# Performance work log

Hardware: AMD Instinct MI355X
Metric: run time of the kernel (lower is better)

The kernel has to match this reference:

```python
import jax, jax.numpy as jnp
import numpy as np
from jax import lax

PAD_IDX = 0
SOS_IDX = 1


def gru_cell(x, h, w_ih, w_hh, b_ih, b_hh):
    # PyTorch GRU cell: gates ordered [r, z, n]
    gi = x @ w_ih.T + b_ih            # [B, 3H]
    gh = h @ w_hh.T + b_hh            # [B, 3H]
    i_r, i_z, i_n = jnp.split(gi, 3, axis=-1)
    h_r, h_z, h_n = jnp.split(gh, 3, axis=-1)
    r = jax.nn.sigmoid(i_r + h_r)
    z = jax.nn.sigmoid(i_z + h_z)
    n = jnp.tanh(i_n + r * h_n)
    return (1.0 - z) * n + z * h


def setup_inputs() -> dict:
    key = jax.random.key(0)
    ks = jax.random.split(key, 24)
    B, S, T = 32, 64, 48
    Vs, Vt, E, H = 32000, 32000, 512, 1024
    sH = 1.0 / np.sqrt(H)
    sE = 1.0 / np.sqrt(E)

    def p(k, shape, scale):
        return jax.random.normal(k, shape, jnp.float32) * scale

    inp = {
        'source_ids': jax.random.randint(ks[0], (B, S), 0, Vs),
        'target_ids': jax.random.randint(ks[1], (B, T), 0, Vt),
        'enc_embed': p(ks[2], (Vs, E), 0.02).at[PAD_IDX].set(0.0),
        'enc_w_ih': p(ks[3], (3 * H, E), sE),
        'enc_w_hh': p(ks[4], (3 * H, H), sH),
        'enc_b_ih': p(ks[5], (3 * H,), sH),
        'enc_b_hh': p(ks[6], (3 * H,), sH),
        'wq': p(ks[7], (H, H), sH),
        'bq': p(ks[8], (H,), sH),
        'wk': p(ks[9], (H, H), sH),
        'bk': p(ks[10], (H,), sH),
        'ws': p(ks[11], (H,), sH),
        'bs': p(ks[12], (), sH),
        'dec_embed': p(ks[13], (Vt, E), 0.02).at[PAD_IDX].set(0.0),
        'dec_w_ih': p(ks[14], (3 * H, E + H), sH),
        'dec_w_hh': p(ks[15], (3 * H, H), sH),
        'dec_b_ih': p(ks[16], (3 * H,), sH),
        'dec_b_hh': p(ks[17], (3 * H,), sH),
        'wo': p(ks[18], (Vt, H), sH),
        'bo': p(ks[19], (Vt,), sH),
    }
    return inp


def reference(source_ids, target_ids, enc_embed, enc_w_ih, enc_w_hh, enc_b_ih,
              enc_b_hh, wq, bq, wk, bk, ws, bs, dec_embed, dec_w_ih, dec_w_hh,
              dec_b_ih, dec_b_hh, wo, bo):
    B, S = source_ids.shape
    T = target_ids.shape[1]
    H = wq.shape[0]

    # ----- encoder GRU -----
    enc_emb = enc_embed[source_ids]                  # [B,S,E] (dropout = identity, eval)
    h0 = jnp.zeros((B, H), enc_emb.dtype)

    def enc_step(h, x):
        h = gru_cell(x, h, enc_w_ih, enc_w_hh, enc_b_ih, enc_b_hh)
        return h, h

    h_final, enc_out = lax.scan(enc_step, h0, enc_emb.transpose(1, 0, 2))
    enc_out = enc_out.transpose(1, 0, 2)             # [B,S,H]

    mask = source_ids != PAD_IDX                     # [B,S]
    keys_proj = enc_out @ wk.T + bk                  # [B,S,H] (hoisted; linear, step-invariant)

    # ----- decoder with teacher forcing (ratio=1.0 => always teacher) -----
    dec_in = jnp.concatenate(
        [jnp.full((B, 1), SOS_IDX, dtype=target_ids.dtype), target_ids[:, 1:T - 1]],
        axis=1)                                      # [B,T-1]
    dec_emb = dec_embed[dec_in].transpose(1, 0, 2)   # [T-1,B,E]

    def dec_step(h, emb):
        q = h @ wq.T + bq                            # [B,H]
        scores = jnp.tanh(q[:, None, :] + keys_proj) @ ws + bs   # [B,S]
        scores = jnp.where(mask, scores, -jnp.inf)
        w = jax.nn.softmax(scores, axis=-1)          # [B,S]
        ctx = jnp.einsum('bs,bsh->bh', w, enc_out)   # [B,H]
        x = jnp.concatenate([emb, ctx], axis=-1)     # [B,E+H]
        h2 = gru_cell(x, h, dec_w_ih, dec_w_hh, dec_b_ih, dec_b_hh)
        logits = h2 @ wo.T + bo                      # [B,V]
        return h2, (logits, w)

    _, (logits, attn) = lax.scan(dec_step, h_final, dec_emb)
    logits = logits.transpose(1, 0, 2)               # [B,T-1,V]
    attn = attn.transpose(1, 0, 2)                   # [B,T-1,S]
    return logits, attn
```

## Files before the change

kernel.cpp:

```cpp
#include <hip/hip_runtime.h>


#define BB 32
#define SS 64
#define TT 48
#define TD 47
#define EE 512
#define HH 1024
#define GG 3072
#define VV 32000
#define SOS_IDX 1
#define MPAD 1536

typedef float f32x4 __attribute__((ext_vector_type(4)));
typedef short bf16x8 __attribute__((ext_vector_type(8)));

static __device__ __forceinline__ float sigmoid_f(float x) {
    return 1.0f / (1.0f + __expf(-x));
}
static __device__ __forceinline__ float tanh_f(float x) {
    return 1.0f - 2.0f / (__expf(2.0f * x) + 1.0f);
}
static __device__ __forceinline__ unsigned short f2bf(float f) {
    unsigned u = __float_as_uint(f);
    u = u + 0x7fffu + ((u >> 16) & 1u);
    return (unsigned short)(u >> 16);
}

__global__ void k_dec_idx(const int* __restrict__ tgt, int* __restrict__ idx) {
    int m = blockIdx.x * 256 + threadIdx.x;
    if (m < TD * BB) {
        int t = m >> 5, b = m & 31;
        idx[m] = (t == 0) ? SOS_IDX : tgt[b * TT + t];
    }
}

__global__ __launch_bounds__(256) void k_gemm128(
    const float* __restrict__ A, const float* __restrict__ Wt,
    const float* __restrict__ bias, float* __restrict__ C,
    const int* __restrict__ rowidx,
    int M, int N, int K, int lda, int ldw, int ldc)
{
    __shared__ __align__(16) float As[16][128];
    __shared__ __align__(16) float Bs[16][128];
    const int tid = threadIdx.x;
    const int tm = tid >> 4, tn = tid & 15;
    const int row0 = blockIdx.y * 128;
    const int col0 = blockIdx.x * 128;
    const int lr = tid >> 1;
    const int lq = tid & 1;

    long arow_off = -1;
    {
        int arow = row0 + lr;
        if (arow < M) {
            int r = rowidx ? rowidx[arow] : arow;
            arow_off = (long)r * lda;
        }
    }
    const long wrow_off = (long)(col0 + lr) * ldw;

    float acc[8][8];
#pragma unroll
    for (int i = 0; i < 8; ++i)
#pragma unroll
        for (int j = 0; j < 8; ++j) acc[i][j] = 0.f;

    for (int k0 = 0; k0 < K; k0 += 16) {
        f32x4 av0 = {0.f,0.f,0.f,0.f}, av1 = {0.f,0.f,0.f,0.f};
        if (arow_off >= 0) {
            av0 = *(const f32x4*)(A + arow_off + k0 + lq * 8);
            av1 = *(const f32x4*)(A + arow_off + k0 + lq * 8 + 4);
        }
        f32x4 wv0 = *(const f32x4*)(Wt + wrow_off + k0 + lq * 8);
        f32x4 wv1 = *(const f32x4*)(Wt + wrow_off + k0 + lq * 8 + 4);
        __syncthreads();
#pragma unroll
        for (int i = 0; i < 4; ++i) {
            As[lq * 8 + i][lr] = av0[i];
            As[lq * 8 + 4 + i][lr] = av1[i];
            Bs[lq * 8 + i][lr] = wv0[i];
            Bs[lq * 8 + 4 + i][lr] = wv1[i];
        }
        __syncthreads();
#pragma unroll
        for (int kk = 0; kk < 16; ++kk) {
            f32x4 a0 = *(const f32x4*)&As[kk][tm * 4];
            f32x4 a1 = *(const f32x4*)&As[kk][64 + tm * 4];
            f32x4 b0 = *(const f32x4*)&Bs[kk][tn * 4];
            f32x4 b1 = *(const f32x4*)&Bs[kk][64 + tn * 4];
            float a[8], b[8];
#pragma unroll
            for (int i = 0; i < 4; ++i) {
                a[i] = a0[i]; a[4 + i] = a1[i];
                b[i] = b0[i]; b[4 + i] = b1[i];
            }
#pragma unroll
            for (int i = 0; i < 8; ++i)
#pragma unroll
                for (int j = 0; j < 8; ++j) acc[i][j] += a[i] * b[j];
        }
    }

    f32x4 bv0 = {0.f,0.f,0.f,0.f}, bv1 = {0.f,0.f,0.f,0.f};
    if (bias) {
        bv0 = *(const f32x4*)(bias + col0 + tn * 4);
        bv1 = *(const f32x4*)(bias + col0 + 64 + tn * 4);
    }
#pragma unroll
    for (int i = 0; i < 8; ++i) {
        int m = row0 + ((i < 4) ? (tm * 4 + i) : (64 + tm * 4 + i - 4));
        if (m >= M) continue;
        f32x4 v0, v1;
#pragma unroll
        for (int j = 0; j < 4; ++j) {
            v0[j] = acc[i][j] + bv0[j];
            v1[j] = acc[i][4 + j] + bv1[j];
        }
        *(f32x4*)(C + (long)m * ldc + col0 + tn * 4) = v0;
        *(f32x4*)(C + (long)m * ldc + col0 + 64 + tn * 4) = v1;
    }
}

__global__ __launch_bounds__(256) void k_cvtA(
    const float* __restrict__ A, unsigned short* __restrict__ Ah,
    unsigned short* __restrict__ Al)
{
    size_t i4 = ((size_t)blockIdx.x * 256 + threadIdx.x) * 4;
    int row = (int)(i4 >> 10);
    f32x4 v = {0.f, 0.f, 0.f, 0.f};
    if (row < TD * BB) v = *(const f32x4*)(A + i4);
    ushort4 h, l;
    float hf;
    h.x = f2bf(v.x); hf = __uint_as_float((unsigned)h.x << 16); l.x = f2bf(v.x - hf);
    h.y = f2bf(v.y); hf = __uint_as_float((unsigned)h.y << 16); l.y = f2bf(v.y - hf);
    h.z = f2bf(v.z); hf = __uint_as_float((unsigned)h.z << 16); l.z = f2bf(v.z - hf);
    h.w = f2bf(v.w); hf = __uint_as_float((unsigned)h.w << 16); l.w = f2bf(v.w - hf);
    *(ushort4*)(Ah + i4) = h;
    *(ushort4*)(Al + i4) = l;
}

__global__ __launch_bounds__(256) void k_cvtB(
    const float* __restrict__ Bsrc, unsigned short* __restrict__ Bh)
{
    size_t i4 = ((size_t)blockIdx.x * 256 + threadIdx.x) * 4;
    f32x4 v = *(const f32x4*)(Bsrc + i4);
    ushort4 h;
    h.x = f2bf(v.x); h.y = f2bf(v.y); h.z = f2bf(v.z); h.w = f2bf(v.w);
    *(ushort4*)(Bh + i4) = h;
}

__global__ __launch_bounds__(256) void k_mfma_logits(
    const unsigned short* __restrict__ Ah,
    const unsigned short* __restrict__ Bh,
    const float* __restrict__ bo, float* __restrict__ C)
{
    __shared__ __align__(16) unsigned short As[128 * 64];
    __shared__ __align__(16) unsigned short Bs[128 * 64];
    const int tid = threadIdx.x;
    const int m0 = blockIdx.y * 128;
    const int n0 = blockIdx.x * 128;
    const int r = tid >> 1, half = tid & 1;
    const int lane = tid & 63, wid = tid >> 6;
    const int wm = wid >> 1, wn = wid & 1;

    f32x4 acc[4][4];
#pragma unroll
    for (int i = 0; i < 4; ++i)
#pragma unroll
        for (int j = 0; j < 4; ++j) acc[i][j] = (f32x4){0.f, 0.f, 0.f, 0.f};

    char* AsB = (char*)As;
    char* BsB = (char*)Bs;
    const int lwb = r * 128 + half * 64;
    const int swz = (r & 7) << 4;

    for (int kt = 0; kt < 32; ++kt) {
        const int kb = (kt & 15) * 64;
        const unsigned short* Ap = Ah + ((kt >> 4) ? (size_t)MPAD * 1024 : 0)
                                 + (size_t)(m0 + r) * 1024 + kb + half * 32;
        const unsigned short* Bp = Bh + (size_t)(n0 + r) * 1024 + kb + half * 32;
        f32x4 a0 = *(const f32x4*)(Ap + 0);
        f32x4 a1 = *(const f32x4*)(Ap + 8);
        f32x4 a2 = *(const f32x4*)(Ap + 16);
        f32x4 a3 = *(const f32x4*)(Ap + 24);
        f32x4 b0 = *(const f32x4*)(Bp + 0);
        f32x4 b1 = *(const f32x4*)(Bp + 8);
        f32x4 b2 = *(const f32x4*)(Bp + 16);
        f32x4 b3 = *(const f32x4*)(Bp + 24);
        __syncthreads();
        *(f32x4*)(AsB + ((lwb + 0)  ^ swz)) = a0;
        *(f32x4*)(AsB + ((lwb + 16) ^ swz)) = a1;
        *(f32x4*)(AsB + ((lwb + 32) ^ swz)) = a2;
        *(f32x4*)(AsB + ((lwb + 48) ^ swz)) = a3;
        *(f32x4*)(BsB + ((lwb + 0)  ^ swz)) = b0;
        *(f32x4*)(BsB + ((lwb + 16) ^ swz)) = b1;
        *(f32x4*)(BsB + ((lwb + 32) ^ swz)) = b2;
        *(f32x4*)(BsB + ((lwb + 48) ^ swz)) = b3;
        __syncthreads();
#pragma unroll
        for (int ks = 0; ks < 2; ++ks) {
            bf16x8 af[4], bf[4];
#pragma unroll
            for (int u = 0; u < 4; ++u) {
                int ml = wm * 64 + u * 16 + (lane & 15);
                int byteA = ml * 128 + ks * 64 + ((lane >> 4) << 4);
                af[u] = *(const bf16x8*)(AsB + (byteA ^ ((ml & 7) << 4)));
                int nl = wn * 64 + u * 16 + (lane & 15);
                int byteB = nl * 128 + ks * 64 + ((lane >> 4) << 4);
                bf[u] = *(const bf16x8*)(BsB + (byteB ^ ((nl & 7) << 4)));
            }
#pragma unroll
            for (int mi = 0; mi < 4; ++mi)
#pragma unroll
                for (int ni = 0; ni < 4; ++ni)
                    acc[mi][ni] = __builtin_amdgcn_mfma_f32_16x16x32_bf16(
                        af[mi], bf[ni], acc[mi][ni], 0, 0, 0);
        }
    }

    const int cl = lane & 15, rq = lane >> 4;
#pragma unroll
    for (int ni = 0; ni < 4; ++ni) {
        int col = n0 + wn * 64 + ni * 16 + cl;
        float bias = bo[col];
#pragma unroll
        for (int mi = 0; mi < 4; ++mi) {
#pragma unroll
            for (int j = 0; j < 4; ++j) {
                int m = m0 + wm * 64 + mi * 16 + rq * 4 + j;
                if (m < TD * BB) {
                    int orow = (m & 31) * TD + (m >> 5);
                    C[(size_t)orow * VV + col] = acc[mi][ni][j] + bias;
                }
            }
        }
    }
}

__global__ __launch_bounds__(512, 2) void k_enc_step(
    const float* __restrict__ gi, const float* __restrict__ Whh,
    const float* __restrict__ bhh, float* __restrict__ enc_out, int s)
{
    __shared__ float red[12][16][32];
    __shared__ float sums[12][32];
    const int tid = threadIdx.x, bid = blockIdx.x;
    const int b = tid & 31, ks = tid >> 5;
    const int j0 = bid * 4;
    const int kc = ks * 64;

    float acc[12];
#pragma unroll
    for (int u = 0; u < 12; ++u) acc[u] = 0.f;
    if (s > 0) {
        f32x4 hreg[16];
        const float* hb = enc_out + ((size_t)b * SS + (s - 1)) * HH + kc;
#pragma unroll
        for (int i = 0; i < 16; ++i) hreg[i] = *(const f32x4*)(hb + (i << 2));
#pragma unroll
        for (int jj = 0; jj < 4; ++jj) {
            const float* pr = Whh + ((size_t)(j0 + jj) << 10) + kc;
            const float* pz = Whh + ((size_t)(HH + j0 + jj) << 10) + kc;
            const float* pn = Whh + ((size_t)(2 * HH + j0 + jj) << 10) + kc;
            float ar = 0.f, az = 0.f, an = 0.f;
#pragma unroll
            for (int i = 0; i < 16; ++i) {
                f32x4 h4 = hreg[i];
                f32x4 w;
                w = *(const f32x4*)(pr + (i << 2));
                ar += h4.x * w.x + h4.y * w.y + h4.z * w.z + h4.w * w.w;
                w = *(const f32x4*)(pz + (i << 2));
                az += h4.x * w.x + h4.y * w.y + h4.z * w.z + h4.w * w.w;
                w = *(const f32x4*)(pn + (i << 2));
                an += h4.x * w.x + h4.y * w.y + h4.z * w.z + h4.w * w.w;
            }
            acc[jj] = ar; acc[4 + jj] = az; acc[8 + jj] = an;
        }
    }
#pragma unroll
    for (int u = 0; u < 12; ++u) red[u][ks][b] = acc[u];
    __syncthreads();
    if (tid < 384) {
        int u = tid >> 5, fb = tid & 31;
        float x = 0.f;
#pragma unroll
        for (int q = 0; q < 16; ++q) x += red[u][q][fb];
        sums[u][fb] = x;
    }
    __syncthreads();
    if (tid < 32) {
        const f32x4 bh0 = *(const f32x4*)(bhh + j0);
        const f32x4 bh1 = *(const f32x4*)(bhh + HH + j0);
        const f32x4 bh2 = *(const f32x4*)(bhh + 2 * HH + j0);
        const float* gr = gi + (size_t)(tid * SS + s) * GG;
        f32x4 g0 = *(const f32x4*)(gr + j0);
        f32x4 g1 = *(const f32x4*)(gr + HH + j0);
        f32x4 g2 = *(const f32x4*)(gr + 2 * HH + j0);
        f32x4 hold = {0.f, 0.f, 0.f, 0.f};
        if (s > 0) hold = *(const f32x4*)(enc_out + ((size_t)tid * SS + (s - 1)) * HH + j0);
        f32x4 hn;
#pragma unroll
        for (int e = 0; e < 4; ++e) {
            float r = sigmoid_f(g0[e] + sums[e][tid] + bh0[e]);
            float z = sigmoid_f(g1[e] + sums[4 + e][tid] + bh1[e]);
            float n = tanh_f(g2[e] + r * (sums[8 + e][tid] + bh2[e]));
            hn[e] = (1.f - z) * n + z * hold[e];
        }
        *(f32x4*)(enc_out + ((size_t)tid * SS + s) * HH + j0) = hn;
    }
}

__global__ __launch_bounds__(512, 2) void k_hq(
    const float* __restrict__ hbase, long hstride,
    const float* __restrict__ Whh, const float* __restrict__ wq,
    const float* __restrict__ bq, float* __restrict__ qbuf,
    float* __restrict__ hsums)
{
    __shared__ float red[16][16][32];
    __shared__ float qsum[4][32];
    const int tid = threadIdx.x, bid = blockIdx.x;
    const int b = tid & 31, ks = tid >> 5;
    const int j0 = bid * 4;
    const int kc = ks * 64;

    f32x4 hreg[16];
    const float* hb = hbase + (size_t)b * hstride + kc;
#pragma unroll
    for (int i = 0; i < 16; ++i) hreg[i] = *(const f32x4*)(hb + (i << 2));
    float acc[16];
#pragma unroll
    for (int jj = 0; jj < 4; ++jj) {
        const float* pr = Whh + ((size_t)(j0 + jj) << 10) + kc;
        const float* pz = Whh + ((size_t)(HH + j0 + jj) << 10) + kc;
        const float* pn = Whh + ((size_t)(2 * HH + j0 + jj) << 10) + kc;
        const float* pq = wq + ((size_t)(j0 + jj) << 10) + kc;
        float ar = 0.f, az = 0.f, an = 0.f, aq = 0.f;
#pragma unroll
        for (int i = 0; i < 16; ++i) {
            f32x4 h4 = hreg[i];
            f32x4 w;
            w = *(const f32x4*)(pr + (i << 2));
            ar += h4.x * w.x + h4.y * w.y + h4.z * w.z + h4.w * w.w;
            w = *(const f32x4*)(pz + (i << 2));
            az += h4.x * w.x + h4.y * w.y + h4.z * w.z + h4.w * w.w;
            w = *(const f32x4*)(pn + (i << 2));
            an += h4.x * w.x + h4.y * w.y + h4.z * w.z + h4.w * w.w;
            w = *(const f32x4*)(pq + (i << 2));
            aq += h4.x * w.x + h4.y * w.y + h4.z * w.z + h4.w * w.w;
        }
        acc[jj] = ar; acc[4 + jj] = az; acc[8 + jj] = an; acc[12 + jj] = aq;
    }
#pragma unroll
    for (int u = 0; u < 16; ++u) red[u][ks][b] = acc[u];
    __syncthreads();
    {
        int u = tid >> 5, fb = tid & 31;
        float x = 0.f;
#pragma unroll
        for (int q = 0; q < 16; ++q) x += red[u][q][fb];
        if (u < 12) {
            int g = u >> 2, jj = u & 3;
            hsums[(size_t)g * BB * HH + (size_t)fb * HH + j0 + jj] = x;
        } else {
            qsum[u - 12][fb] = x;
        }
    }
    __syncthreads();
    if (tid < 32) {
        const f32x4 bq4 = *(const f32x4*)(bq + j0);
        f32x4 qv;
        qv.x = qsum[0][tid] + bq4.x;
        qv.y = qsum[1][tid] + bq4.y;
        qv.z = qsum[2][tid] + bq4.z;
        qv.w = qsum[3][tid] + bq4.w;
        *(f32x4*)(qbuf + (size_t)tid * HH + j0) = qv;
    }
}

__global__ __launch_bounds__(512, 2) void k_attn_fin(
    const float* __restrict__ qbuf, const float* __restrict__ keys,
    const float* __restrict__ wsv, const float* __restrict__ bsv,
    const int* __restrict__ src, const float* __restrict__ encproj,
    const float* __restrict__ gi, const float* __restrict__ bhh,
    const float* __restrict__ hsums, const float* __restrict__ hbase,
    long hstride, float* __restrict__ h2all, float* __restrict__ attn_out,
    int t)
{
    __shared__ float qs[HH];
    __shared__ float wss[HH];
    __shared__ float sc[8][64];
    __shared__ float wl[64];
    __shared__ float xls[GG];
    const int ab = blockIdx.x;
    const int tid = threadIdx.x;
    if (tid < 256) {
        *(f32x4*)&qs[tid * 4] = *(const f32x4*)(qbuf + (size_t)ab * HH + tid * 4);
        *(f32x4*)&wss[tid * 4] = *(const f32x4*)(wsv + tid * 4);
    }
    __syncthreads();
    {
        const int s4 = tid >> 3, kq = tid & 7;
        const float* kr = keys + (size_t)(ab * SS + s4) * HH + kq * 128;
        float a = 0.f;
        for (int i = 0; i < 32; ++i) {
            f32x4 kv = *(const f32x4*)(kr + (i << 2));
            int k = kq * 128 + (i << 2);
            a += tanh_f(qs[k] + kv.x) * wss[k]
               + tanh_f(qs[k + 1] + kv.y) * wss[k + 1]
               + tanh_f(qs[k + 2] + kv.z) * wss[k + 2]
               + tanh_f(qs[k + 3] + kv.w) * wss[k + 3];
        }
        sc[kq][s4] = a;
    }
    __syncthreads();
    if (tid < 64) {
        float v = bsv[0];
#pragma unroll
        for (int q = 0; q < 8; ++q) v += sc[q][tid];
        bool valid = src[ab * SS + tid] != 0;
        float m = valid ? v : -3.0e38f;
        for (int off = 32; off; off >>= 1) m = fmaxf(m, __shfl_xor(m, off));
        float e = valid ? __expf(v - m) : 0.f;
        float ssum = e;
        for (int off = 32; off; off >>= 1) ssum += __shfl_xor(ssum, off);
        float wgt = e / ssum;
        wl[tid] = wgt;
        attn_out[((size_t)ab * TD + t) * SS + tid] = wgt;
    }
    __syncthreads();
    {
        float xa[6] = {0.f, 0.f, 0.f, 0.f, 0.f, 0.f};
        for (int s2 = 0; s2 < SS; ++s2) {
            float wgt = wl[s2];
            const float* ep = encproj + (size_t)(ab * SS + s2) * GG;
#pragma unroll
            for (int u = 0; u < 6; ++u)
                xa[u] += wgt * ep[u * 512 + tid];
        }
#pragma unroll
        for (int u = 0; u < 6; ++u) xls[u * 512 + tid] = xa[u];
    }
    __syncthreads();
    const float* gr = gi + (size_t)(t * BB + ab) * GG;
#pragma unroll
    for (int half = 0; half < 2; ++half) {
        int j = half * 512 + tid;
        float g0 = gr[j] + xls[j];
        float g1 = gr[HH + j] + xls[HH + j];
        float g2 = gr[2 * HH + j] + xls[2 * HH + j];
        float sh0 = hsums[(size_t)0 * BB * HH + (size_t)ab * HH + j];
        float sh1 = hsums[(size_t)1 * BB * HH + (size_t)ab * HH + j];
        float sh2 = hsums[(size_t)2 * BB * HH + (size_t)ab * HH + j];
        float r = sigmoid_f(g0 + sh0 + bhh[j]);
        float z = sigmoid_f(g1 + sh1 + bhh[HH + j]);
        float n = tanh_f(g2 + r * (sh2 + bhh[2 * HH + j]));
        float hold = hbase[(size_t)ab * hstride + j];
        h2all[((size_t)t * BB + ab) * HH + j] = (1.f - z) * n + z * hold;
    }
}

extern "C" void kernel_launch(void* const* d_in, const int* in_sizes, int n_in,
                              void* d_out, int out_size, void* d_ws, size_t ws_size,
                              hipStream_t stream)
{
    const int*   src  = (const int*)d_in[0];
    const int*   tgt  = (const int*)d_in[1];
    const float* eemb = (const float*)d_in[2];
    const float* ewih = (const float*)d_in[3];
    const float* ewhh = (const float*)d_in[4];
    const float* ebih = (const float*)d_in[5];
    const float* ebhh = (const float*)d_in[6];
    const float* wq   = (const float*)d_in[7];
    const float* bq   = (const float*)d_in[8];
    const float* wk   = (const float*)d_in[9];
    const float* bk   = (const float*)d_in[10];
    const float* wsv  = (const float*)d_in[11];
    const float* bsv  = (const float*)d_in[12];
    const float* demb = (const float*)d_in[13];
    const float* dwih = (const float*)d_in[14];
    const float* dwhh = (const float*)d_in[15];
    const float* dbih = (const float*)d_in[16];
    const float* dbhh = (const float*)d_in[17];
    const float* wo   = (const float*)d_in[18];
    const float* bo   = (const float*)d_in[19];
    float* out = (float*)d_out;

    float* w = (float*)d_ws;
    float* enc_gi  = w;
    float* dec_gi  = enc_gi  + (size_t)BB * SS * GG;
    float* enc_out = dec_gi  + (size_t)TD * BB * GG;
    float* keys    = enc_out + (size_t)BB * SS * HH;
    float* h2all   = keys    + (size_t)BB * SS * HH;
    float* qbuf    = h2all   + (size_t)TD * BB * HH;
    float* hsums   = qbuf    + (size_t)BB * HH;
    int*   didx    = (int*)(hsums + (size_t)3 * BB * HH);
    unsigned short* Ah = (unsigned short*)(didx + TD * BB + 32);
    unsigned short* Al = Ah + (size_t)MPAD * 1024;
    unsigned short* Bh = (unsigned short*)w;

    float* encproj = enc_gi;
    float* attn_out = out + (size_t)BB * TD * VV;

    k_dec_idx<<<dim3((TD * BB + 255) / 256), 256, 0, stream>>>(tgt, didx);

    k_gemm128<<<dim3(GG / 128, (BB * SS) / 128), 256, 0, stream>>>(
        eemb, ewih, ebih, enc_gi, src, BB * SS, GG, EE, EE, EE, GG);
    k_gemm128<<<dim3(GG / 128, (TD * BB + 127) / 128), 256, 0, stream>>>(
        demb, dwih, dbih, dec_gi, didx, TD * BB, GG, EE, EE, EE + HH, GG);

    for (int s = 0; s < SS; ++s)
        k_enc_step<<<dim3(256), dim3(512), 0, stream>>>(
            enc_gi, ewhh, ebhh, enc_out, s);

    k_gemm128<<<dim3(HH / 128, (BB * SS) / 128), 256, 0, stream>>>(
        enc_out, wk, bk, keys, nullptr, BB * SS, HH, HH, HH, HH, HH);
    k_gemm128<<<dim3(GG / 128, (BB * SS) / 128), 256, 0, stream>>>(
        enc_out, dwih + EE, nullptr, encproj, nullptr,
        BB * SS, GG, HH, HH, EE + HH, GG);

    for (int t = 0; t < TD; ++t) {
        const float* hbase = (t == 0) ? enc_out + (size_t)(SS - 1) * HH
                                      : h2all + (size_t)(t - 1) * BB * HH;
        long hstride = (t == 0) ? (long)SS * HH : (long)HH;
        k_hq<<<dim3(256), dim3(512), 0, stream>>>(
            hbase, hstride, dwhh, wq, bq, qbuf, hsums);
        k_attn_fin<<<dim3(BB), dim3(512), 0, stream>>>(
            qbuf, keys, wsv, bsv, src, encproj, dec_gi, dbhh, hsums,
            hbase, hstride, h2all, attn_out, t);
    }

    k_cvtA<<<dim3(MPAD * 1024 / 1024), 256, 0, stream>>>(h2all, Ah, Al);
    k_cvtB<<<dim3(VV * 1024 / 1024), 256, 0, stream>>>(wo, Bh);
    k_mfma_logits<<<dim3(VV / 128, MPAD / 128), 256, 0, stream>>>(
        Ah, Bh, bo, out);
}
```

Measured before the change: 4.495 ms.

## Fuse recurrent steps with software grid barriers and merge decoder kernels

Batches four encoder GRU steps per launch, separated by a hierarchical atomic grid barrier, which cuts the encoder from 64 launches to 16. The decoder's two per-step kernels (h/q projection and attention+GRU finish) become one 256-block kernel with a grid barrier between them. The attention and gate stage is spread over 256 blocks instead of 32: each block handles one batch row and a 128-column slice, and the softmax is recomputed redundantly in every slice. Cross-block stores use sc0/sc1 cache-bypassing instructions for coherence. The barrier relies on all 256 blocks being co-resident, and deadlocks if they are not.

```diff
diff --git a/kernel.cpp b/kernel.cpp
--- a/kernel.cpp
+++ b/kernel.cpp
@@ -25,6 +25,31 @@
     unsigned u = __float_as_uint(f);
     u = u + 0x7fffu + ((u >> 16) & 1u);
     return (unsigned short)(u >> 16);
+}
+static __device__ __forceinline__ void cst4(float* p, f32x4 v) {
+    asm volatile("global_store_dwordx4 %0, %1, off sc0 sc1" :: "v"(p), "v"(v) : "memory");
+}
+static __device__ __forceinline__ void cst1(float* p, float v) {
+    asm volatile("global_store_dword %0, %1, off sc0 sc1" :: "v"(p), "v"(v) : "memory");
+}
+
+static __device__ __forceinline__ void gbar(int* bar, int leafsz, int& bstep) {
+    asm volatile("s_waitcnt vmcnt(0) lgkmcnt(0)" ::: "memory");
+    __syncthreads();
+    bstep += 1;
+    if (threadIdx.x == 0) {
+        int* leaf = bar + (blockIdx.x & 7) * 32;
+        int* root = bar + 512;
+        int lv = __hip_atomic_fetch_add(leaf, 1, __ATOMIC_RELAXED, __HIP_MEMORY_SCOPE_AGENT) + 1;
+        if (lv == bstep * leafsz) {
+            __hip_atomic_fetch_add(root, 1, __ATOMIC_RELAXED, __HIP_MEMORY_SCOPE_AGENT);
+        }
+        while (__hip_atomic_load(root, __ATOMIC_RELAXED, __HIP_MEMORY_SCOPE_AGENT) < bstep * 8) {
+            __builtin_amdgcn_s_sleep(1);
+        }
+    }
+    __syncthreads();
+    asm volatile("" ::: "memory");
 }
 
 __global__ void k_dec_idx(const int* __restrict__ tgt, int* __restrict__ idx) {
@@ -238,9 +263,10 @@
     }
 }
 
-__global__ __launch_bounds__(512, 2) void k_enc_step(
+__global__ __launch_bounds__(512, 2) void k_enc_steps(
     const float* __restrict__ gi, const float* __restrict__ Whh,
-    const float* __restrict__ bhh, float* __restrict__ enc_out, int s)
+    const float* __restrict__ bhh, float* __restrict__ enc_out,
+    int s0, int ns, int* bar)
 {
     __shared__ float red[12][16][32];
     __shared__ float sums[12][32];
@@ -248,21 +274,105 @@
     const int b = tid & 31, ks = tid >> 5;
     const int j0 = bid * 4;
     const int kc = ks * 64;
-
-    float acc[12];
-#pragma unroll
-    for (int u = 0; u < 12; ++u) acc[u] = 0.f;
-    if (s > 0) {
+    int bstep = 0;
+
+    for (int ss = 0; ss < ns; ++ss) {
+        const int s = s0 + ss;
+        float acc[12];
+#pragma unroll
+        for (int u = 0; u < 12; ++u) acc[u] = 0.f;
+        if (s > 0) {
+            f32x4 hreg[16];
+            const float* hb = enc_out + ((size_t)b * SS + (s - 1)) * HH + kc;
+#pragma unroll
+            for (int i = 0; i < 16; ++i) hreg[i] = *(const f32x4*)(hb + (i << 2));
+#pragma unroll
+            for (int jj = 0; jj < 4; ++jj) {
+                const float* pr = Whh + ((size_t)(j0 + jj) << 10) + kc;
+                const float* pz = Whh + ((size_t)(HH + j0 + jj) << 10) + kc;
+                const float* pn = Whh + ((size_t)(2 * HH + j0 + jj) << 10) + kc;
+                float ar = 0.f, az = 0.f, an = 0.f;
+#pragma unroll
+                for (int i = 0; i < 16; ++i) {
+                    f32x4 h4 = hreg[i];
+                    f32x4 w;
+                    w = *(const f32x4*)(pr + (i << 2));
+                    ar += h4.x * w.x + h4.y * w.y + h4.z * w.z + h4.w * w.w;
+                    w = *(const f32x4*)(pz + (i << 2));
+                    az += h4.x * w.x + h4.y * w.y + h4.z * w.z + h4.w * w.w;
+                    w = *(const f32x4*)(pn + (i << 2));
+                    an += h4.x * w.x + h4.y * w.y + h4.z * w.z + h4.w * w.w;
+                }
+                acc[jj] = ar; acc[4 + jj] = az; acc[8 + jj] = an;
+            }
+        }
+#pragma unroll
+        for (int u = 0; u < 12; ++u) red[u][ks][b] = acc[u];
+        __syncthreads();
+        if (tid < 384) {
+            int u = tid >> 5, fb = tid & 31;
+            float x = 0.f;
+#pragma unroll
+            for (int q = 0; q < 16; ++q) x += red[u][q][fb];
+            sums[u][fb] = x;
+        }
+        __syncthreads();
+        if (tid < 32) {
+            const f32x4 bh0 = *(const f32x4*)(bhh + j0);
+            const f32x4 bh1 = *(const f32x4*)(bhh + HH + j0);
+            const f32x4 bh2 = *(const f32x4*)(bhh + 2 * HH + j0);
+            const float* gr = gi + (size_t)(tid * SS + s) * GG;
+            f32x4 g0 = *(const f32x4*)(gr + j0);
+            f32x4 g1 = *(const f32x4*)(gr + HH + j0);
+            f32x4 g2 = *(const f32x4*)(gr + 2 * HH + j0);
+            f32x4 hold = {0.f, 0.f, 0.f, 0.f};
+            if (s > 0) hold = *(const f32x4*)(enc_out + ((size_t)tid * SS + (s - 1)) * HH + j0);
+            f32x4 hn;
+#pragma unroll
+            for (int e = 0; e < 4; ++e) {
+                float r = sigmoid_f(g0[e] + sums[e][tid] + bh0[e]);
+                float z = sigmoid_f(g1[e] + sums[4 + e][tid] + bh1[e]);
+                float n = tanh_f(g2[e] + r * (sums[8 + e][tid] + bh2[e]));
+                hn[e] = (1.f - z) * n + z * hold[e];
+            }
+            cst4(enc_out + ((size_t)tid * SS + s) * HH + j0, hn);
+        }
+        if (ss != ns - 1) gbar(bar, 256 / 8, bstep);
+    }
+}
+
+__global__ __launch_bounds__(512, 2) void k_dec_step(
+    const float* __restrict__ hbase, long hstride,
+    const float* __restrict__ Whh, const float* __restrict__ wq,
+    const float* __restrict__ bq, const float* __restrict__ keys,
+    const float* __restrict__ wsv, const float* __restrict__ bsv,
+    const int* __restrict__ src, const float* __restrict__ encproj,
+    const float* __restrict__ gi, const float* __restrict__ bhh,
+    float* __restrict__ q2, float* __restrict__ hsums2,
+    float* __restrict__ h2all, float* __restrict__ attn_out,
+    int t, int* bar)
+{
+    __shared__ float red[16][16][32];
+    __shared__ float qsum[4][32];
+    const int tid = threadIdx.x, bid = blockIdx.x;
+    const int b = tid & 31, ks = tid >> 5;
+    const int j0 = bid * 4;
+    const int kc = ks * 64;
+    int bstep = 0;
+
+    {
         f32x4 hreg[16];
-        const float* hb = enc_out + ((size_t)b * SS + (s - 1)) * HH + kc;
+        const float* hb = hbase + (size_t)b * hstride + kc;
 #pragma unroll
         for (int i = 0; i < 16; ++i) hreg[i] = *(const f32x4*)(hb + (i << 2));
+        float acc[16];
 #pragma unroll
         for (int jj = 0; jj < 4; ++jj) {
             const float* pr = Whh + ((size_t)(j0 + jj) << 10) + kc;
             const float* pz = Whh + ((size_t)(HH + j0 + jj) << 10) + kc;
             const float* pn = Whh + ((size_t)(2 * HH + j0 + jj) << 10) + kc;
-            float ar = 0.f, az = 0.f, an = 0.f;
+            const float* pq = wq + ((size_t)(j0 + jj) << 10) + kc;
+            float ar = 0.f, az = 0.f, an = 0.f, aq = 0.f;
 #pragma unroll
             for (int i = 0; i < 16; ++i) {
                 f32x4 h4 = hreg[i];
@@ -273,129 +383,46 @@
                 az += h4.x * w.x + h4.y * w.y + h4.z * w.z + h4.w * w.w;
                 w = *(const f32x4*)(pn + (i << 2));
                 an += h4.x * w.x + h4.y * w.y + h4.z * w.z + h4.w * w.w;
+                w = *(const f32x4*)(pq + (i << 2));
+                aq += h4.x * w.x + h4.y * w.y + h4.z * w.z + h4.w * w.w;
             }
-            acc[jj] = ar; acc[4 + jj] = az; acc[8 + jj] = an;
-        }
-    }
-#pragma unroll
-    for (int u = 0; u < 12; ++u) red[u][ks][b] = acc[u];
-    __syncthreads();
-    if (tid < 384) {
-        int u = tid >> 5, fb = tid & 31;
-        float x = 0.f;
-#pragma unroll
-        for (int q = 0; q < 16; ++q) x += red[u][q][fb];
-        sums[u][fb] = x;
-    }
-    __syncthreads();
-    if (tid < 32) {
-        const f32x4 bh0 = *(const f32x4*)(bhh + j0);
-        const f32x4 bh1 = *(const f32x4*)(bhh + HH + j0);
-        const f32x4 bh2 = *(const f32x4*)(bhh + 2 * HH + j0);
-        const float* gr = gi + (size_t)(tid * SS + s) * GG;
-        f32x4 g0 = *(const f32x4*)(gr + j0);
-        f32x4 g1 = *(const f32x4*)(gr + HH + j0);
-        f32x4 g2 = *(const f32x4*)(gr + 2 * HH + j0);
-        f32x4 hold = {0.f, 0.f, 0.f, 0.f};
-        if (s > 0) hold = *(const f32x4*)(enc_out + ((size_t)tid * SS + (s - 1)) * HH + j0);
-        f32x4 hn;
-#pragma unroll
-        for (int e = 0; e < 4; ++e) {
-            float r = sigmoid_f(g0[e] + sums[e][tid] + bh0[e]);
-            float z = sigmoid_f(g1[e] + sums[4 + e][tid] + bh1[e]);
-            float n = tanh_f(g2[e] + r * (sums[8 + e][tid] + bh2[e]));
-            hn[e] = (1.f - z) * n + z * hold[e];
-        }
-        *(f32x4*)(enc_out + ((size_t)tid * SS + s) * HH + j0) = hn;
-    }
-}
-
-__global__ __launch_bounds__(512, 2) void k_hq(
-    const float* __restrict__ hbase, long hstride,
-    const float* __restrict__ Whh, const float* __restrict__ wq,
-    const float* __restrict__ bq, float* __restrict__ qbuf,
-    float* __restrict__ hsums)
-{
-    __shared__ float red[16][16][32];
-    __shared__ float qsum[4][32];
-    const int tid = threadIdx.x, bid = blockIdx.x;
-    const int b = tid & 31, ks = tid >> 5;
-    const int j0 = bid * 4;
-    const int kc = ks * 64;
-
-    f32x4 hreg[16];
-    const float* hb = hbase + (size_t)b * hstride + kc;
-#pragma unroll
-    for (int i = 0; i < 16; ++i) hreg[i] = *(const f32x4*)(hb + (i << 2));
-    float acc[16];
-#pragma unroll
-    for (int jj = 0; jj < 4; ++jj) {
-        const float* pr = Whh + ((size_t)(j0 + jj) << 10) + kc;
-        const float* pz = Whh + ((size_t)(HH + j0 + jj) << 10) + kc;
-        const float* pn = Whh + ((size_t)(2 * HH + j0 + jj) << 10) + kc;
-        const float* pq = wq + ((size_t)(j0 + jj) << 10) + kc;
-        float ar = 0.f, az = 0.f, an = 0.f, aq = 0.f;
-#pragma unroll
-        for (int i = 0; i < 16; ++i) {
-            f32x4 h4 = hreg[i];
-            f32x4 w;
-            w = *(const f32x4*)(pr + (i << 2));
-            ar += h4.x * w.x + h4.y * w.y + h4.z * w.z + h4.w * w.w;
-            w = *(const f32x4*)(pz + (i << 2));
-            az += h4.x * w.x + h4.y * w.y + h4.z * w.z + h4.w * w.w;
-            w = *(const f32x4*)(pn + (i << 2));
-            an += h4.x * w.x + h4.y * w.y + h4.z * w.z + h4.w * w.w;
-            w = *(const f32x4*)(pq + (i << 2));
-            aq += h4.x * w.x + h4.y * w.y + h4.z * w.z + h4.w * w.w;
-        }
-        acc[jj] = ar; acc[4 + jj] = az; acc[8 + jj] = an; acc[12 + jj] = aq;
-    }
-#pragma unroll
-    for (int u = 0; u < 16; ++u) red[u][ks][b] = acc[u];
-    __syncthreads();
-    {
-        int u = tid >> 5, fb = tid & 31;
-        float x = 0.f;
-#pragma unroll
-        for (int q = 0; q < 16; ++q) x += red[u][q][fb];
-        if (u < 12) {
-            int g = u >> 2, jj = u & 3;
-            hsums[(size_t)g * BB * HH + (size_t)fb * HH + j0 + jj] = x;
-        } else {
-            qsum[u - 12][fb] = x;
-        }
-    }
-    __syncthreads();
-    if (tid < 32) {
-        const f32x4 bq4 = *(const f32x4*)(bq + j0);
-        f32x4 qv;
-        qv.x = qsum[0][tid] + bq4.x;
-        qv.y = qsum[1][tid] + bq4.y;
-        qv.z = qsum[2][tid] + bq4.z;
-        qv.w = qsum[3][tid] + bq4.w;
-        *(f32x4*)(qbuf + (size_t)tid * HH + j0) = qv;
-    }
-}
-
-__global__ __launch_bounds__(512, 2) void k_attn_fin(
-    const float* __restrict__ qbuf, const float* __restrict__ keys,
-    const float* __restrict__ wsv, const float* __restrict__ bsv,
-    const int* __restrict__ src, const float* __restrict__ encproj,
-    const float* __restrict__ gi, const float* __restrict__ bhh,
-    const float* __restrict__ hsums, const float* __restrict__ hbase,
-    long hstride, float* __restrict__ h2all, float* __restrict__ attn_out,
-    int t)
-{
-    __shared__ float qs[HH];
-    __shared__ float wss[HH];
-    __shared__ float sc[8][64];
-    __shared__ float wl[64];
-    __shared__ float xls[GG];
-    const int ab = blockIdx.x;
-    const int tid = threadIdx.x;
+            acc[jj] = ar; acc[4 + jj] = az; acc[8 + jj] = an; acc[12 + jj] = aq;
+        }
+#pragma unroll
+        for (int u = 0; u < 16; ++u) red[u][ks][b] = acc[u];
+        __syncthreads();
+        {
+            int u = tid >> 5, fb = tid & 31;
+            float x = 0.f;
+#pragma unroll
+            for (int q = 0; q < 16; ++q) x += red[u][q][fb];
+            if (u < 12) cst1(hsums2 + (size_t)bid * 384 + u * 32 + fb, x);
+            else qsum[u - 12][fb] = x;
+        }
+        __syncthreads();
+        if (tid < 32) {
+            const f32x4 bq4 = *(const f32x4*)(bq + j0);
+            f32x4 qv;
+            qv.x = qsum[0][tid] + bq4.x;
+            qv.y = qsum[1][tid] + bq4.y;
+            qv.z = qsum[2][tid] + bq4.z;
+            qv.w = qsum[3][tid] + bq4.w;
+            cst4(q2 + (size_t)bid * 128 + tid * 4, qv);
+        }
+    }
+    gbar(bar, 256 / 8, bstep);
+
+    const int ab = bid & 31, part = bid >> 5;
+    float* qs  = &red[0][0][0];
+    float* wss = qs + 1024;
+    float* scs = wss + 1024;
+    float* wl  = scs + 512;
+    float* xls = wl + 64;
     if (tid < 256) {
-        *(f32x4*)&qs[tid * 4] = *(const f32x4*)(qbuf + (size_t)ab * HH + tid * 4);
-        *(f32x4*)&wss[tid * 4] = *(const f32x4*)(wsv + tid * 4);
+        f32x4 qv = *(const f32x4*)(q2 + (size_t)tid * 128 + ab * 4);
+        f32x4 wv = *(const f32x4*)(wsv + tid * 4);
+        *(f32x4*)&qs[tid * 4] = qv;
+        *(f32x4*)&wss[tid * 4] = wv;
     }
     __syncthreads();
     {
@@ -410,13 +437,13 @@
                + tanh_f(qs[k + 2] + kv.z) * wss[k + 2]
                + tanh_f(qs[k + 3] + kv.w) * wss[k + 3];
         }
-        sc[kq][s4] = a;
+        scs[kq * 64 + s4] = a;
     }
     __syncthreads();
     if (tid < 64) {
         float v = bsv[0];
 #pragma unroll
-        for (int q = 0; q < 8; ++q) v += sc[q][tid];
+        for (int q = 0; q < 8; ++q) v += scs[q * 64 + tid];
         bool valid = src[ab * SS + tid] != 0;
         float m = valid ? v : -3.0e38f;
         for (int off = 32; off; off >>= 1) m = fmaxf(m, __shfl_xor(m, off));
@@ -425,35 +452,32 @@
         for (int off = 32; off; off >>= 1) ssum += __shfl_xor(ssum, off);
         float wgt = e / ssum;
         wl[tid] = wgt;
-        attn_out[((size_t)ab * TD + t) * SS + tid] = wgt;
+        if (part == 0)
+            attn_out[((size_t)ab * TD + t) * SS + tid] = wgt;
     }
     __syncthreads();
-    {
-        float xa[6] = {0.f, 0.f, 0.f, 0.f, 0.f, 0.f};
-        for (int s2 = 0; s2 < SS; ++s2) {
-            float wgt = wl[s2];
-            const float* ep = encproj + (size_t)(ab * SS + s2) * GG;
-#pragma unroll
-            for (int u = 0; u < 6; ++u)
-                xa[u] += wgt * ep[u * 512 + tid];
-        }
-#pragma unroll
-        for (int u = 0; u < 6; ++u) xls[u * 512 + tid] = xa[u];
+    if (tid < 384) {
+        int gate = tid >> 7, jj = tid & 127;
+        int col = (gate << 10) + (part << 7) + jj;
+        float xa = 0.f;
+        const float* ep = encproj + (size_t)ab * SS * GG + col;
+        for (int s2 = 0; s2 < 64; ++s2)
+            xa += wl[s2] * ep[(size_t)s2 * GG];
+        xls[tid] = xa;
     }
     __syncthreads();
-    const float* gr = gi + (size_t)(t * BB + ab) * GG;
-#pragma unroll
-    for (int half = 0; half < 2; ++half) {
-        int j = half * 512 + tid;
-        float g0 = gr[j] + xls[j];
-        float g1 = gr[HH + j] + xls[HH + j];
-        float g2 = gr[2 * HH + j] + xls[2 * HH + j];
-        float sh0 = hsums[(size_t)0 * BB * HH + (size_t)ab * HH + j];
-        float sh1 = hsums[(size_t)1 * BB * HH + (size_t)ab * HH + j];
-        float sh2 = hsums[(size_t)2 * BB * HH + (size_t)ab * HH + j];
-        float r = sigmoid_f(g0 + sh0 + bhh[j]);
-        float z = sigmoid_f(g1 + sh1 + bhh[HH + j]);
-        float n = tanh_f(g2 + r * (sh2 + bhh[2 * HH + j]));
+    if (tid < 128) {
+        const int j = (part << 7) + tid;
+        const int wbid = (part << 5) + (tid >> 2);
+        const int jj = tid & 3;
+        const float* hs = hsums2 + (size_t)wbid * 384;
+        float sh0 = hs[(0 * 4 + jj) * 32 + ab];
+        float sh1 = hs[(1 * 4 + jj) * 32 + ab];
+        float sh2 = hs[(2 * 4 + jj) * 32 + ab];
+        const float* gr = gi + (size_t)(t * BB + ab) * GG;
+        float r = sigmoid_f(gr[j] + xls[tid] + sh0 + bhh[j]);
+        float z = sigmoid_f(gr[HH + j] + xls[128 + tid] + sh1 + bhh[HH + j]);
+        float n = tanh_f(gr[2 * HH + j] + xls[256 + tid] + r * (sh2 + bhh[2 * HH + j]));
         float hold = hbase[(size_t)ab * hstride + j];
         h2all[((size_t)t * BB + ab) * HH + j] = (1.f - z) * n + z * hold;
     }
@@ -491,16 +515,18 @@
     float* enc_out = dec_gi  + (size_t)TD * BB * GG;
     float* keys    = enc_out + (size_t)BB * SS * HH;
     float* h2all   = keys    + (size_t)BB * SS * HH;
-    float* qbuf    = h2all   + (size_t)TD * BB * HH;
-    float* hsums   = qbuf    + (size_t)BB * HH;
-    int*   didx    = (int*)(hsums + (size_t)3 * BB * HH);
-    unsigned short* Ah = (unsigned short*)(didx + TD * BB + 32);
+    float* q2      = h2all   + (size_t)TD * BB * HH;
+    float* hsums2  = q2      + (size_t)256 * 128;
+    int*   didx    = (int*)(hsums2 + (size_t)256 * 384);
+    int*   barAll  = didx + TD * BB + 32;
+    unsigned short* Ah = (unsigned short*)(barAll + 63 * 576 + 32);
     unsigned short* Al = Ah + (size_t)MPAD * 1024;
     unsigned short* Bh = (unsigned short*)w;
 
     float* encproj = enc_gi;
     float* attn_out = out + (size_t)BB * TD * VV;
 
+    hipMemsetAsync(barAll, 0, 63 * 576 * sizeof(int), stream);
     k_dec_idx<<<dim3((TD * BB + 255) / 256), 256, 0, stream>>>(tgt, didx);
 
     k_gemm128<<<dim3(GG / 128, (BB * SS) / 128), 256, 0, stream>>>(
@@ -508,9 +534,9 @@
     k_gemm128<<<dim3(GG / 128, (TD * BB + 127) / 128), 256, 0, stream>>>(
         demb, dwih, dbih, dec_gi, didx, TD * BB, GG, EE, EE, EE + HH, GG);
 
-    for (int s = 0; s < SS; ++s)
-        k_enc_step<<<dim3(256), dim3(512), 0, stream>>>(
-            enc_gi, ewhh, ebhh, enc_out, s);
+    for (int i = 0; i < 16; ++i)
+        k_enc_steps<<<dim3(256), dim3(512), 0, stream>>>(
+            enc_gi, ewhh, ebhh, enc_out, i * 4, 4, barAll + i * 576);
 
     k_gemm128<<<dim3(HH / 128, (BB * SS) / 128), 256, 0, stream>>>(
         enc_out, wk, bk, keys, nullptr, BB * SS, HH, HH, HH, HH, HH);
@@ -522,11 +548,9 @@
         const float* hbase = (t == 0) ? enc_out + (size_t)(SS - 1) * HH
                                       : h2all + (size_t)(t - 1) * BB * HH;
         long hstride = (t == 0) ? (long)SS * HH : (long)HH;
-        k_hq<<<dim3(256), dim3(512), 0, stream>>>(
-            hbase, hstride, dwhh, wq, bq, qbuf, hsums);
-        k_attn_fin<<<dim3(BB), dim3(512), 0, stream>>>(
-            qbuf, keys, wsv, bsv, src, encproj, dec_gi, dbhh, hsums,
-            hbase, hstride, h2all, attn_out, t);
+        k_dec_step<<<dim3(256), dim3(512), 0, stream>>>(
+            hbase, hstride, dwhh, wq, bq, keys, wsv, bsv, src, encproj,
+            dec_gi, dbhh, q2, hsums2, h2all, attn_out, t, barAll + (16 + t) * 576);
     }
 
     k_cvtA<<<dim3(MPAD * 1024 / 1024), 256, 0, stream>>>(h2all, Ah, Al);
```

New measurement: 4.588 ms. 2.1% more time.
